# Optimization experiments

Hardware: AMD Instinct MI355X
Metric: run time of the kernel (lower is better)

## Reference

```python
import jax, jax.numpy as jnp
import numpy as np

R_MAX = 32
S_MAX = 2
C_Z = 128
IN_DIM = 4 * R_MAX + 2 * S_MAX + 7  # 139
B, N = 1, 1024


def setup_inputs() -> dict:
    key = jax.random.key(0)
    ks = jax.random.split(key, 6)
    asym_id = jnp.sort(jax.random.randint(ks[0], (B, N), 0, 4), axis=-1)
    residue_index = jnp.sort(jax.random.randint(ks[1], (B, N), 0, 512), axis=-1)
    entity_id = jnp.sort(jax.random.randint(ks[2], (B, N), 0, 3), axis=-1)
    sym_id = jax.random.randint(ks[3], (B, N), 0, 3)
    token_index = jnp.sort(jax.random.randint(ks[4], (B, N), 0, 1024), axis=-1)
    W = jax.random.normal(ks[5], (IN_DIM, C_Z), dtype=jnp.float32) * 0.02
    return {"asym_id": asym_id, "residue_index": residue_index,
            "entity_id": entity_id, "sym_id": sym_id,
            "token_index": token_index, "W": W}


def reference(asym_id, residue_index, entity_id, sym_id, token_index, W):
    # Pairwise same-chain / same-residue / same-entity masks: [B, N, N]
    same_chain = asym_id[..., :, None] == asym_id[..., None, :]
    same_res = residue_index[..., :, None] == residue_index[..., None, :]
    same_ent = entity_id[..., :, None] == entity_id[..., None, :]

    # Clipped relative indices (values in [0, 2*r_max+1] / [0, 2*s_max+1])
    d_res = jnp.where(
        same_chain,
        jnp.clip(residue_index[..., :, None] - residue_index[..., None, :] + R_MAX, 0, 2 * R_MAX),
        2 * R_MAX + 1)
    d_tok = jnp.where(
        same_chain & same_res,
        jnp.clip(token_index[..., :, None] - token_index[..., None, :] + R_MAX, 0, 2 * R_MAX),
        2 * R_MAX + 1)
    d_chain = jnp.where(
        same_ent,
        jnp.clip(sym_id[..., :, None] - sym_id[..., None, :] + S_MAX, 0, 2 * S_MAX),
        2 * S_MAX + 1)

    # concat(one_hot(d_res,66), one_hot(d_tok,66), same_ent, one_hot(d_chain,6)) @ W
    # == sum of gathered weight rows: avoids materializing the [B,N,N,139] one-hot.
    n_pos = 2 * (R_MAX + 1)          # 66
    W_pos = W[:n_pos]                # rows 0..65
    W_tok = W[n_pos:2 * n_pos]       # rows 66..131
    w_ent = W[2 * n_pos]             # row 132
    W_chn = W[2 * n_pos + 1:]        # rows 133..138

    p = (W_pos[d_res] + W_tok[d_tok]
         + same_ent[..., None].astype(W.dtype) * w_ent
         + W_chn[d_chain])           # [B, N, N, c_z]
    return p
```

## Files before the change

### kernel.cpp

```cpp
#include <hip/hip_runtime.h>


typedef float f4 __attribute__((ext_vector_type(4)));

constexpr int kN     = 1024;
constexpr int kRowF4 = 32;
constexpr int kWF4   = 139 * kRowF4;

__global__ __launch_bounds__(1024) void relpos_kernel(
    const int* __restrict__ asym,
    const int* __restrict__ resi,
    const int* __restrict__ ent,
    const int* __restrict__ sym,
    const int* __restrict__ tok,
    const float* __restrict__ W,
    float* __restrict__ out)
{
    __shared__ f4  sW[kWF4];
    __shared__ int sKey[kN];

    const int tid = threadIdx.x;
    const f4* __restrict__ W4 = reinterpret_cast<const f4*>(W);

    for (int idx = tid; idx < kWF4; idx += 1024) {
        f4 v = W4[idx];
        if (idx >= 133 * kRowF4 && idx < 138 * kRowF4)
            v += W4[132 * kRowF4 + (idx & (kRowF4 - 1))];
        sW[idx] = v;
    }
    {
        const int j = tid;
        sKey[j] = (asym[j] & 3) | ((ent[j] & 3) << 2) | ((sym[j] & 3) << 4)
                | ((resi[j] & 511) << 6) | ((tok[j] & 1023) << 15);
    }
    __syncthreads();

    const int c4 = tid & 31;
    const int jg = tid >> 5;

    f4* __restrict__ out4 = reinterpret_cast<f4*>(out);

    const int i0 = blockIdx.x * 2;
    for (int ii = 0; ii < 2; ++ii) {
        const int i = i0 + ii;
        const int ai = asym[i], ri = resi[i], ei = ent[i], si = sym[i], ti = tok[i];
        f4* __restrict__ orow = out4 + (size_t)i * kN * kRowF4 + c4;

        for (int it = 0; it < kN / 32; ++it) {
            const int j = it * 32 + jg;
            const int k = sKey[j];
            const int aj =  k        & 3;
            const int ej = (k >> 2)  & 3;
            const int sj = (k >> 4)  & 3;
            const int rj = (k >> 6)  & 511;
            const int tj = (k >> 15) & 1023;

            const bool same_chain = (ai == aj);
            const bool same_ent   = (ei == ej);

            int dres = min(max(ri - rj + 32, 0), 64);
            if (!same_chain) dres = 65;
            int dtok = min(max(ti - tj + 32, 0), 64);
            if (!(same_chain && (ri == rj))) dtok = 65;
            int dchn = min(max(si - sj + 2, 0), 4);
            if (!same_ent) dchn = 5;

            const f4 wa = sW[dres * kRowF4 + c4];
            const f4 wb = sW[(66 + dtok) * kRowF4 + c4];
            const f4 wc = sW[(133 + dchn) * kRowF4 + c4];

            orow[(size_t)j * kRowF4] = wa + wb + wc;
        }
    }
}

extern "C" void kernel_launch(void* const* d_in, const int* in_sizes, int n_in,
                              void* d_out, int out_size, void* d_ws, size_t ws_size,
                              hipStream_t stream) {
    const int*   asym = (const int*)d_in[0];
    const int*   resi = (const int*)d_in[1];
    const int*   ent  = (const int*)d_in[2];
    const int*   sym  = (const int*)d_in[3];
    const int*   tok  = (const int*)d_in[4];
    const float* W    = (const float*)d_in[5];
    float*       out  = (float*)d_out;

    relpos_kernel<<<dim3(kN / 2), dim3(1024), 0, stream>>>(asym, resi, ent, sym, tok, W, out);
}
```

Before: 101.4 us.

## Grid-stride output over wave-sized chunks instead of per-block row pairs

Result: slower. 117.8 us (+16.2%).

```diff
diff --git a/kernel.cpp b/kernel.cpp
--- a/kernel.cpp
+++ b/kernel.cpp
@@ -3,11 +3,15 @@
 
 typedef float f4 __attribute__((ext_vector_type(4)));
 
-constexpr int kN     = 1024;
-constexpr int kRowF4 = 32;
-constexpr int kWF4   = 139 * kRowF4;
+constexpr int kN      = 1024;
+constexpr int kRowF4  = 32;
+constexpr int kWF4    = 139 * kRowF4;
+constexpr int kThr    = 1024;
+constexpr int kBlocks = 512;
+constexpr int kWaves  = kBlocks * (kThr / 64);
+constexpr int kChunks = kN * kN * kRowF4 / 64;
 
-__global__ __launch_bounds__(1024) void relpos_kernel(
+__global__ __launch_bounds__(kThr) void relpos_kernel(
     const int* __restrict__ asym,
     const int* __restrict__ resi,
     const int* __restrict__ ent,
@@ -22,7 +26,7 @@
     const int tid = threadIdx.x;
     const f4* __restrict__ W4 = reinterpret_cast<const f4*>(W);
 
-    for (int idx = tid; idx < kWF4; idx += 1024) {
+    for (int idx = tid; idx < kWF4; idx += kThr) {
         f4 v = W4[idx];
         if (idx >= 133 * kRowF4 && idx < 138 * kRowF4)
             v += W4[132 * kRowF4 + (idx & (kRowF4 - 1))];
@@ -35,42 +39,40 @@
     }
     __syncthreads();
 
-    const int c4 = tid & 31;
-    const int jg = tid >> 5;
+    const int lane = tid & 63;
+    const int c4   = lane & 31;
+    const int jh   = lane >> 5;
 
     f4* __restrict__ out4 = reinterpret_cast<f4*>(out);
 
-    const int i0 = blockIdx.x * 2;
-    for (int ii = 0; ii < 2; ++ii) {
-        const int i = i0 + ii;
-        const int ai = asym[i], ri = resi[i], ei = ent[i], si = sym[i], ti = tok[i];
-        f4* __restrict__ orow = out4 + (size_t)i * kN * kRowF4 + c4;
+    const int gw = blockIdx.x * (kThr / 64) + (tid >> 6);
 
-        for (int it = 0; it < kN / 32; ++it) {
-            const int j = it * 32 + jg;
-            const int k = sKey[j];
-            const int aj =  k        & 3;
-            const int ej = (k >> 2)  & 3;
-            const int sj = (k >> 4)  & 3;
-            const int rj = (k >> 6)  & 511;
-            const int tj = (k >> 15) & 1023;
+    #pragma unroll 2
+    for (int c = gw; c < kChunks; c += kWaves) {
+        const int i = c >> 9;
+        const int j = ((c & 511) << 1) | jh;
 
-            const bool same_chain = (ai == aj);
-            const bool same_ent   = (ei == ej);
+        const int ki = sKey[i];
+        const int kj = sKey[j];
 
-            int dres = min(max(ri - rj + 32, 0), 64);
-            if (!same_chain) dres = 65;
-            int dtok = min(max(ti - tj + 32, 0), 64);
-            if (!(same_chain && (ri == rj))) dtok = 65;
-            int dchn = min(max(si - sj + 2, 0), 4);
-            if (!same_ent) dchn = 5;
+        const int ai =  ki        & 3, aj =  kj        & 3;
+        const int ei = (ki >> 2)  & 3, ej = (kj >> 2)  & 3;
+        const int si = (ki >> 4)  & 3, sj = (kj >> 4)  & 3;
+        const int ri = (ki >> 6)  & 511, rj = (kj >> 6)  & 511;
+        const int ti = (ki >> 15) & 1023, tj = (kj >> 15) & 1023;
 
-            const f4 wa = sW[dres * kRowF4 + c4];
-            const f4 wb = sW[(66 + dtok) * kRowF4 + c4];
-            const f4 wc = sW[(133 + dchn) * kRowF4 + c4];
+        int dres = min(max(ri - rj + 32, 0), 64);
+        if (ai != aj) dres = 65;
+        int dtok = min(max(ti - tj + 32, 0), 64);
+        if (!(ai == aj && ri == rj)) dtok = 65;
+        int dchn = min(max(si - sj + 2, 0), 4);
+        if (ei != ej) dchn = 5;
 
-            orow[(size_t)j * kRowF4] = wa + wb + wc;
-        }
+        const f4 v = sW[dres * kRowF4 + c4]
+                   + sW[(66 + dtok) * kRowF4 + c4]
+                   + sW[(133 + dchn) * kRowF4 + c4];
+
+        out4[(size_t)c * 64 + lane] = v;
     }
 }
 
@@ -85,5 +87,5 @@
     const float* W    = (const float*)d_in[5];
     float*       out  = (float*)d_out;
 
-    relpos_kernel<<<dim3(kN / 2), dim3(1024), 0, stream>>>(asym, resi, ent, sym, tok, W, out);
+    relpos_kernel<<<dim3(kBlocks), dim3(kThr), 0, stream>>>(asym, resi, ent, sym, tok, W, out);
 }
```
